# Kernel optimization log

Hardware: AMD Instinct MI355X
Metric: run time of the kernel (lower is better)

The kernel has to match this reference:

```python
import jax, jax.numpy as jnp
import numpy as np


def setup_inputs() -> dict:
    key = jax.random.key(0)
    k1, k2 = jax.random.split(key)
    B, N, M = 16, 4096, 4096
    x1 = jax.random.normal(k1, (B, N, 3), dtype=jnp.float32)
    x2 = jax.random.normal(k2, (B, M, 3), dtype=jnp.float32)
    return {"x1": x1, "x2": x2}


def reference(x1, x2) -> jnp.ndarray:
    # x1: [B, N, 3], x2: [B, M, 3]
    # dist_matrix[b, i, j] = ||x1[b,i] - x2[b,j]||^2 via |a|^2 + |b|^2 - 2 a.b
    x1_norm = jnp.sum(x1 * x1, axis=2, keepdims=True)           # [B, N, 1]
    x2_norm = jnp.sum(x2 * x2, axis=2)[:, None, :]              # [B, 1, M]
    cross = jnp.einsum('bnd,bmd->bnm', x1, x2)                  # [B, N, M]
    dist_matrix = x1_norm + x2_norm - 2.0 * cross               # [B, N, M]
    min_1_to_2 = jnp.min(dist_matrix, axis=2)                   # [B, N]
    min_2_to_1 = jnp.min(dist_matrix, axis=1)                   # [B, M]
    chamfer = jnp.mean(min_1_to_2, axis=1) + jnp.mean(min_2_to_1, axis=1)  # [B]
    return chamfer
```

## Files before the change

### kernel.cpp

```cpp
#include <hip/hip_runtime.h>


typedef __attribute__((ext_vector_type(8))) __bf16 bf16x8;
typedef __attribute__((ext_vector_type(16))) float f32x16;

#define PTS 4096
#define TILES 128
#define NB 16

__device__ __forceinline__ unsigned f2bf(float f) {
  unsigned u = __float_as_uint(f);
  return (u + 0x7FFFu + ((u >> 16) & 1u)) >> 16;
}
__device__ __forceinline__ float bf2f(unsigned s) {
  return __uint_as_float(s << 16);
}
__device__ __forceinline__ unsigned pk(unsigned lo, unsigned hi) {
  return (lo & 0xFFFFu) | (hi << 16);
}

__global__ __launch_bounds__(256) void prepack_b(const float* __restrict__ x1,
                                                 const float* __restrict__ x2,
                                                 uint4* __restrict__ Bfr,
                                                 unsigned* __restrict__ rowm,
                                                 float* __restrict__ out) {
  const int id = blockIdx.x * 256 + threadIdx.x;
  rowm[id] = 0x7F800000u;
  if (id < NB) out[id] = 0.f;
  const int d = id >> 16;
  const int b = (id >> 12) & (NB - 1);
  const int j = id & (PTS - 1);
  const float* q = (d ? x1 : x2) + (size_t)(b * PTS + j) * 3;
  const float x = q[0], y = q[1], z = q[2];
  const float sx = -2.f * x, sy = -2.f * y, sz = -2.f * z;
  const unsigned Hx = f2bf(sx), Hy = f2bf(sy), Hz = f2bf(sz);
  const unsigned Lx = f2bf(sx - bf2f(Hx));
  const unsigned Ly = f2bf(sy - bf2f(Hy));
  const unsigned Lz = f2bf(sz - bf2f(Hz));
  const float n = fmaf(x, x, fmaf(y, y, z * z));
  const unsigned nh = f2bf(n), nl = f2bf(n - bf2f(nh));
  const unsigned one = 0x3F80u;
  uint4 w0, w1;
  w0.x = pk(Hx, Hy); w0.y = pk(Hz, Lx); w0.z = pk(Ly, Lz); w0.w = pk(Hx, Hy);
  w1.x = pk(Hz, nh); w1.y = pk(nl, one); w1.z = pk(one, 0u); w1.w = 0u;
  uint4* base =
      Bfr + ((size_t)((d * NB + b) * TILES + (j >> 5)) * 2) * 32 + (j & 31);
  base[0]  = w0;
  base[32] = w1;
}

__global__ __launch_bounds__(256, 4) void chamfer_main(
    const float* __restrict__ x1, const float* __restrict__ x2,
    const uint4* __restrict__ Bfr, unsigned* __restrict__ rowm) {
  const int s  = blockIdx.x;
  const int d  = s & 1;
  const int b  = (s >> 1) & (NB - 1);
  const int cq = (s >> 5) & 3;
  const int rg = blockIdx.y;

  const int tid  = threadIdx.x;
  const int lane = tid & 63;
  const int half = lane >> 5;
  const int l31  = lane & 31;
  const int wave = tid >> 6;

  __shared__ uint4 lds[2048];

  const uint4* bp = Bfr + ((size_t)((d * NB + b) * TILES + cq * 32) * 2) * 32;
#pragma unroll
  for (int k = 0; k < 8; ++k) lds[tid + k * 256] = bp[tid + k * 256];

  const float* P = d ? x2 : x1;
  const int t0 = rg * 8 + wave * 2;
  bf16x8 af[2];
#pragma unroll
  for (int rr = 0; rr < 2; ++rr) {
    const int r = (t0 + rr) * 32 + l31;
    const float* p = P + (size_t)(b * PTS + r) * 3;
    const float x = p[0], y = p[1], zc = p[2];
    const unsigned hx = f2bf(x), hy = f2bf(y), hz = f2bf(zc);
    const unsigned lx = f2bf(x - bf2f(hx));
    const unsigned ly = f2bf(y - bf2f(hy));
    const unsigned lz = f2bf(zc - bf2f(hz));
    const float n = fmaf(x, x, fmaf(y, y, zc * zc));
    const unsigned nh = f2bf(n), nl = f2bf(n - bf2f(nh));
    const unsigned one = 0x3F80u;
    uint4 w0, w1;
    w0.x = pk(hx, hy); w0.y = pk(hz, hx); w0.z = pk(hy, hz); w0.w = pk(lx, ly);
    w1.x = pk(lz, one); w1.y = pk(one, nh); w1.z = pk(nl, 0u); w1.w = 0u;
    uint4 w;
    w.x = half ? w1.x : w0.x; w.y = half ? w1.y : w0.y;
    w.z = half ? w1.z : w0.z; w.w = half ? w1.w : w0.w;
    af[rr] = *(const bf16x8*)&w;
  }
  const bf16x8 af0 = af[0], af1 = af[1];

  f32x16 zero;
#pragma unroll
  for (int e = 0; e < 16; ++e) zero[e] = 0.f;

  float rm0[16], rm1[16];
#pragma unroll
  for (int e = 0; e < 16; ++e) { rm0[e] = 3.0e38f; rm1[e] = 3.0e38f; }

  __syncthreads();

  const uint4* tp = &lds[half * 32 + l31];
  bf16x8 buf[4];
  buf[0] = *(const bf16x8*)&tp[0];
  buf[1] = *(const bf16x8*)&tp[64];

#pragma unroll 2
  for (int g = 0; g < 16; ++g) {
    const int cur = (g & 1) * 2;
    const int nxt = ((g + 1) & 1) * 2;
    const int pf  = ((g + 1) & 15) * 2;
    buf[nxt]     = *(const bf16x8*)&tp[pf * 64];
    buf[nxt + 1] = *(const bf16x8*)&tp[(pf + 1) * 64];
    const bf16x8 b0 = buf[cur], b1 = buf[cur + 1];
    const f32x16 a00 =
        __builtin_amdgcn_mfma_f32_32x32x16_bf16(af0, b0, zero, 0, 0, 0);
    const f32x16 a01 =
        __builtin_amdgcn_mfma_f32_32x32x16_bf16(af0, b1, zero, 0, 0, 0);
#pragma unroll
    for (int e = 0; e < 16; ++e)
      rm0[e] = fminf(fminf(a00[e], a01[e]), rm0[e]);
    const f32x16 a10 =
        __builtin_amdgcn_mfma_f32_32x32x16_bf16(af1, b0, zero, 0, 0, 0);
    const f32x16 a11 =
        __builtin_amdgcn_mfma_f32_32x32x16_bf16(af1, b1, zero, 0, 0, 0);
#pragma unroll
    for (int e = 0; e < 16; ++e)
      rm1[e] = fminf(fminf(a10[e], a11[e]), rm1[e]);
  }

  unsigned* rbase = rowm + (size_t)(d * NB + b) * PTS + t0 * 32;
#pragma unroll
  for (int e = 0; e < 16; ++e) {
    float v = rm0[e];
    v = fminf(v, __shfl_xor(v, 1));
    v = fminf(v, __shfl_xor(v, 2));
    v = fminf(v, __shfl_xor(v, 4));
    v = fminf(v, __shfl_xor(v, 8));
    v = fminf(v, __shfl_xor(v, 16));
    if (l31 == e) {
      const int rl = (e & 3) + 8 * (e >> 2) + 4 * half;
      atomicMin(rbase + rl, __float_as_uint(fmaxf(v, 0.f)));
    }
  }
#pragma unroll
  for (int e = 0; e < 16; ++e) {
    float v = rm1[e];
    v = fminf(v, __shfl_xor(v, 1));
    v = fminf(v, __shfl_xor(v, 2));
    v = fminf(v, __shfl_xor(v, 4));
    v = fminf(v, __shfl_xor(v, 8));
    v = fminf(v, __shfl_xor(v, 16));
    if (l31 == e) {
      const int rl = 32 + (e & 3) + 8 * (e >> 2) + 4 * half;
      atomicMin(rbase + rl, __float_as_uint(fmaxf(v, 0.f)));
    }
  }
}

__global__ __launch_bounds__(256) void reduce_rows(
    const unsigned* __restrict__ rowm, float* __restrict__ out) {
  const int b = blockIdx.x >> 2;
  const int seg = blockIdx.x & 3;
  const int tid = threadIdx.x;
  const unsigned* r0 = rowm + (size_t)b * PTS + seg * 1024;
  const unsigned* r1 = rowm + (size_t)(NB + b) * PTS + seg * 1024;
  float s = 0.f;
  for (int i = tid; i < 1024; i += 256)
    s += __uint_as_float(r0[i]) + __uint_as_float(r1[i]);
  s += __shfl_xor(s, 1);
  s += __shfl_xor(s, 2);
  s += __shfl_xor(s, 4);
  s += __shfl_xor(s, 8);
  s += __shfl_xor(s, 16);
  s += __shfl_xor(s, 32);
  __shared__ float acc[4];
  if ((tid & 63) == 0) acc[tid >> 6] = s;
  __syncthreads();
  if (tid == 0)
    atomicAdd(&out[b], (acc[0] + acc[1] + acc[2] + acc[3]) * (1.f / PTS));
}

extern "C" void kernel_launch(void* const* d_in, const int* in_sizes, int n_in,
                              void* d_out, int out_size, void* d_ws,
                              size_t ws_size, hipStream_t stream) {
  const float* x1 = (const float*)d_in[0];
  const float* x2 = (const float*)d_in[1];
  float* out = (float*)d_out;

  uint4* Bfr = (uint4*)d_ws;
  unsigned* rowm =
      (unsigned*)((char*)d_ws + (size_t)2 * NB * TILES * 2 * 32 * 16);

  prepack_b<<<(2 * NB * PTS) / 256, 256, 0, stream>>>(x1, x2, Bfr, rowm, out);
  dim3 grid(128, NB);
  chamfer_main<<<grid, 256, 0, stream>>>(x1, x2, Bfr, rowm);
  reduce_rows<<<64, 256, 0, stream>>>(rowm, out);
}
```

Measured before the change: 94.65 us.

## Fuse column prepacking into main kernel and enlarge blocks to 512 threads

Removes the separate prepack kernel. Each block now converts its 2048-point column chunk into the bf16 hi/lo fragment layout directly in LDS, instead of reading a prepacked global buffer. Blocks grow to 8 waves covering 16 row tiles, and each wave loops over twice as many column tiles, so there are fewer blocks and fewer atomicMin writes. The row-min and output buffers are now initialised with hipMemsetAsync. In exchange, the packing is recomputed redundantly by every row group, and LDS per block doubles to 64KB, which limits occupancy.

Measured after the change: 84.09 us. 11.2% less time.

```diff
diff --git a/kernel.cpp b/kernel.cpp
--- a/kernel.cpp
+++ b/kernel.cpp
@@ -5,7 +5,6 @@
 typedef __attribute__((ext_vector_type(16))) float f32x16;
 
 #define PTS 4096
-#define TILES 128
 #define NB 16
 
 __device__ __forceinline__ unsigned f2bf(float f) {
@@ -19,43 +18,13 @@
   return (lo & 0xFFFFu) | (hi << 16);
 }
 
-__global__ __launch_bounds__(256) void prepack_b(const float* __restrict__ x1,
-                                                 const float* __restrict__ x2,
-                                                 uint4* __restrict__ Bfr,
-                                                 unsigned* __restrict__ rowm,
-                                                 float* __restrict__ out) {
-  const int id = blockIdx.x * 256 + threadIdx.x;
-  rowm[id] = 0x7F800000u;
-  if (id < NB) out[id] = 0.f;
-  const int d = id >> 16;
-  const int b = (id >> 12) & (NB - 1);
-  const int j = id & (PTS - 1);
-  const float* q = (d ? x1 : x2) + (size_t)(b * PTS + j) * 3;
-  const float x = q[0], y = q[1], z = q[2];
-  const float sx = -2.f * x, sy = -2.f * y, sz = -2.f * z;
-  const unsigned Hx = f2bf(sx), Hy = f2bf(sy), Hz = f2bf(sz);
-  const unsigned Lx = f2bf(sx - bf2f(Hx));
-  const unsigned Ly = f2bf(sy - bf2f(Hy));
-  const unsigned Lz = f2bf(sz - bf2f(Hz));
-  const float n = fmaf(x, x, fmaf(y, y, z * z));
-  const unsigned nh = f2bf(n), nl = f2bf(n - bf2f(nh));
-  const unsigned one = 0x3F80u;
-  uint4 w0, w1;
-  w0.x = pk(Hx, Hy); w0.y = pk(Hz, Lx); w0.z = pk(Ly, Lz); w0.w = pk(Hx, Hy);
-  w1.x = pk(Hz, nh); w1.y = pk(nl, one); w1.z = pk(one, 0u); w1.w = 0u;
-  uint4* base =
-      Bfr + ((size_t)((d * NB + b) * TILES + (j >> 5)) * 2) * 32 + (j & 31);
-  base[0]  = w0;
-  base[32] = w1;
-}
-
-__global__ __launch_bounds__(256, 4) void chamfer_main(
+__global__ __launch_bounds__(512, 2) void chamfer_main(
     const float* __restrict__ x1, const float* __restrict__ x2,
-    const uint4* __restrict__ Bfr, unsigned* __restrict__ rowm) {
+    unsigned* __restrict__ rowm) {
   const int s  = blockIdx.x;
   const int d  = s & 1;
   const int b  = (s >> 1) & (NB - 1);
-  const int cq = (s >> 5) & 3;
+  const int ch = (s >> 5) & 1;
   const int rg = blockIdx.y;
 
   const int tid  = threadIdx.x;
@@ -64,14 +33,32 @@
   const int l31  = lane & 31;
   const int wave = tid >> 6;
 
-  __shared__ uint4 lds[2048];
+  __shared__ uint4 lds[4096];
 
-  const uint4* bp = Bfr + ((size_t)((d * NB + b) * TILES + cq * 32) * 2) * 32;
+  const float* Q = d ? x1 : x2;
+  const int cbase = b * PTS + ch * 2048;
 #pragma unroll
-  for (int k = 0; k < 8; ++k) lds[tid + k * 256] = bp[tid + k * 256];
+  for (int k = 0; k < 4; ++k) {
+    const int j = tid + k * 512;
+    const float* q = Q + (size_t)(cbase + j) * 3;
+    const float x = q[0], y = q[1], z = q[2];
+    const float sx = -2.f * x, sy = -2.f * y, sz = -2.f * z;
+    const unsigned Hx = f2bf(sx), Hy = f2bf(sy), Hz = f2bf(sz);
+    const unsigned Lx = f2bf(sx - bf2f(Hx));
+    const unsigned Ly = f2bf(sy - bf2f(Hy));
+    const unsigned Lz = f2bf(sz - bf2f(Hz));
+    const float n = fmaf(x, x, fmaf(y, y, z * z));
+    const unsigned nh = f2bf(n), nl = f2bf(n - bf2f(nh));
+    const unsigned one = 0x3F80u;
+    uint4 w0, w1;
+    w0.x = pk(Hx, Hy); w0.y = pk(Hz, Lx); w0.z = pk(Ly, Lz); w0.w = pk(Hx, Hy);
+    w1.x = pk(Hz, nh); w1.y = pk(nl, one); w1.z = pk(one, 0u); w1.w = 0u;
+    lds[(j >> 5) * 64 + (j & 31)]      = w0;
+    lds[(j >> 5) * 64 + 32 + (j & 31)] = w1;
+  }
 
   const float* P = d ? x2 : x1;
-  const int t0 = rg * 8 + wave * 2;
+  const int t0 = rg * 16 + wave * 2;
   bf16x8 af[2];
 #pragma unroll
   for (int rr = 0; rr < 2; ++rr) {
@@ -111,10 +98,10 @@
   buf[1] = *(const bf16x8*)&tp[64];
 
 #pragma unroll 2
-  for (int g = 0; g < 16; ++g) {
+  for (int g = 0; g < 32; ++g) {
     const int cur = (g & 1) * 2;
     const int nxt = ((g + 1) & 1) * 2;
-    const int pf  = ((g + 1) & 15) * 2;
+    const int pf  = ((g + 1) & 31) * 2;
     buf[nxt]     = *(const bf16x8*)&tp[pf * 64];
     buf[nxt + 1] = *(const bf16x8*)&tp[(pf + 1) * 64];
     const bf16x8 b0 = buf[cur], b1 = buf[cur + 1];
@@ -193,12 +180,12 @@
   const float* x2 = (const float*)d_in[1];
   float* out = (float*)d_out;
 
-  uint4* Bfr = (uint4*)d_ws;
-  unsigned* rowm =
-      (unsigned*)((char*)d_ws + (size_t)2 * NB * TILES * 2 * 32 * 16);
+  unsigned* rowm = (unsigned*)d_ws;
 
-  prepack_b<<<(2 * NB * PTS) / 256, 256, 0, stream>>>(x1, x2, Bfr, rowm, out);
-  dim3 grid(128, NB);
-  chamfer_main<<<grid, 256, 0, stream>>>(x1, x2, Bfr, rowm);
+  hipMemsetAsync(rowm, 0x7F, (size_t)2 * NB * PTS * 4, stream);
+  hipMemsetAsync(out, 0, NB * sizeof(float), stream);
+
+  dim3 grid(64, 8);
+  chamfer_main<<<grid, 512, 0, stream>>>(x1, x2, rowm);
   reduce_rows<<<64, 256, 0, stream>>>(rowm, out);
 }
```
